# Kernel tuning notes

Hardware: AMD Instinct MI355X
Metric: run time of the kernel (lower is better)

## Reference

```python
import jax, jax.numpy as jnp
import numpy as np

WB = 8   # weight bit width (signed int8, power-of-two scale)
AB = 8   # activation bit width (uint8, power-of-two scale)
BB = 8   # bias bit width

# (name, c_in, c_out, kernel) for every QuantConv2d in order
_CFG = [("1", 3, 32, 3), ("2", 32, 16, 3), ("31", 16, 16, 1), ("32", 16, 32, 3),
        ("33", 32, 32, 1), ("34", 32, 64, 3), ("41", 64, 32, 1), ("42", 32, 64, 3),
        ("43", 64, 32, 1), ("44", 32, 64, 3), ("45", 64, 32, 1), ("46", 32, 64, 3)]
_POOL_AFTER = {"1", "2", "34"}  # MaxPool2d(2,2) follows these blocks


def _ste_round(x):
    # straight-through rounding (Brevitas-style fake quant)
    return x + jax.lax.stop_gradient(jnp.round(x) - x)


def _p2_scale(maxv, levels):
    # power-of-two (fixed point) per-tensor scale covering maxv with `levels` steps
    maxv = jnp.maximum(jax.lax.stop_gradient(maxv), 1e-8)
    return 2.0 ** jnp.ceil(jnp.log2(maxv / levels))


def quant_int(x, bw):
    # signed symmetric fixed-point fake quant (Int8WeightPerTensorFixedPoint style)
    n = 2.0 ** (bw - 1) - 1.0
    s = _p2_scale(jnp.max(jnp.abs(x)), n)
    return jnp.clip(_ste_round(x / s), -n - 1.0, n) * s


def quant_uint(x, bw):
    # unsigned fixed-point fake quant (Uint8ActPerTensorFixedPoint style)
    n = 2.0 ** bw - 1.0
    s = _p2_scale(jnp.max(x), n)
    return jnp.clip(_ste_round(x / s), 0.0, n) * s


def _conv(x, w, pad):
    return jax.lax.conv_general_dilated(
        x, w, window_strides=(1, 1), padding=[(pad, pad), (pad, pad)],
        dimension_numbers=("NCHW", "OIHW", "NCHW"))


def _maxpool2(x):
    return jax.lax.reduce_window(x, -jnp.inf, jax.lax.max,
                                 (1, 1, 2, 2), (1, 1, 2, 2), "VALID")


def _forward(x, p):
    # QuantIdentity on input (uint8 fixed point)
    x = quant_uint(x, AB)
    for n, ci, co, k in _CFG:
        pad = (k - 1) // 2
        y = _conv(x, quant_int(p["w" + n], WB), pad)               # quantized conv, no bias
        # BatchNorm2dToQuantScaleBias: per-channel affine with quantized scale/bias
        y = (y * quant_int(p["sg" + n], WB)[None, :, None, None]
             + quant_int(p["sb" + n], BB)[None, :, None, None])
        x = quant_uint(jax.nn.relu(y), AB)                          # QuantReLU
        if n in _POOL_AFTER:
            x = _maxpool2(x)
    # TruncAvgPool2d(28,28) over the remaining 28x28 map + RoundTo8bit requant
    x = quant_uint(jnp.mean(x, axis=(2, 3)), 8)                     # [B, 64]
    h = x @ quant_int(p["fw1"], WB).T + quant_int(p["fb1"], BB)     # linear51
    h = quant_uint(jax.nn.relu(h), AB)                              # relu5
    return h @ quant_int(p["fw2"], WB).T + quant_int(p["fb2"], BB)  # linear52


def setup_inputs() -> dict:
    key = jax.random.key(0)
    ks = iter(jax.random.split(key, 64))
    inp = {"x": jax.random.uniform(next(ks), (16, 3, 224, 224), jnp.float32)}
    for n, ci, co, k in _CFG:
        inp["w" + n] = jax.random.normal(next(ks), (co, ci, k, k), jnp.float32) * 0.1
        inp["sg" + n] = jax.random.uniform(next(ks), (co,), jnp.float32, 0.5, 1.5)
        inp["sb" + n] = jax.random.normal(next(ks), (co,), jnp.float32) * 0.1
    inp["fw1"] = jax.random.normal(next(ks), (16, 64), jnp.float32) * 0.1
    inp["fb1"] = jax.random.normal(next(ks), (16,), jnp.float32) * 0.1
    inp["fw2"] = jax.random.normal(next(ks), (10, 16), jnp.float32) * 0.1
    inp["fb2"] = jax.random.normal(next(ks), (10,), jnp.float32) * 0.1
    return inp


def reference(x, w1, sg1, sb1, w2, sg2, sb2, w31, sg31, sb31, w32, sg32, sb32,
              w33, sg33, sb33, w34, sg34, sb34, w41, sg41, sb41, w42, sg42, sb42,
              w43, sg43, sb43, w44, sg44, sb44, w45, sg45, sb45, w46, sg46, sb46,
              fw1, fb1, fw2, fb2):
    p = dict(locals())
    x = p.pop("x")
    return _forward(x, p)
```

## Files before the change

### kernel.cpp

```cpp
#include <hip/hip_runtime.h>
#include <math.h>

#define NL 12

typedef short v8s __attribute__((ext_vector_type(8)));
typedef float v4f __attribute__((ext_vector_type(4)));

struct PrepArgs {
  const float* in[40];
  void* out[40];
  int n[40];
  int mode[40];
  int tc[40];
  int ci[40], kk[40], kp[40], co[40];
};

__device__ inline float p2_scale_f(float maxv, float levels) {
  float r = __fdiv_rn(fmaxf(maxv, 1e-8f), levels);
  unsigned b = __float_as_uint(r);
  unsigned e = (b >> 23) & 0xffu;
  e += (b & 0x7fffffu) ? 1u : 0u;
  return __uint_as_float(e << 23);
}

__device__ inline float p2_inv(float s) {
  return __uint_as_float((254u << 23) - __float_as_uint(s));
}

__device__ inline float block_reduce_max256(float v) {
  __shared__ float sm[4];
  #pragma unroll
  for (int off = 32; off; off >>= 1) v = fmaxf(v, __shfl_down(v, off));
  if ((threadIdx.x & 63) == 0) sm[threadIdx.x >> 6] = v;
  __syncthreads();
  if (threadIdx.x == 0) v = fmaxf(fmaxf(sm[0], sm[1]), fmaxf(sm[2], sm[3]));
  return v;
}

__device__ inline void slot_max_update(float* slot, float v) {
  volatile unsigned int* su = (volatile unsigned int*)slot;
  unsigned int bits = __float_as_uint(v);
  if (bits > *su) atomicMax((unsigned int*)slot, bits);
}

__device__ inline short ibf16(float v) {
  return (short)(__float_as_uint(v) >> 16);
}

__global__ void prep_kernel(PrepArgs a, float* wslot,
                            const float* __restrict__ x, int nx, float* slot0) {
  if (blockIdx.x >= 40) {
    const float4* xv = (const float4*)x;
    const int nv = nx >> 2;
    float m0 = 0.f, m1 = 0.f, m2 = 0.f, m3 = 0.f;
    for (int i = (blockIdx.x - 40) * 256 + threadIdx.x; i < nv;
         i += (gridDim.x - 40) * 256) {
      float4 v = xv[i];
      m0 = fmaxf(m0, v.x); m1 = fmaxf(m1, v.y);
      m2 = fmaxf(m2, v.z); m3 = fmaxf(m3, v.w);
    }
    float m = fmaxf(fmaxf(m0, m1), fmaxf(m2, m3));
    float bm = block_reduce_max256(m);
    if (threadIdx.x == 0) slot_max_update(slot0, bm);
    return;
  }
  __shared__ float ssc;
  const int t = blockIdx.x;
  const float* in = a.in[t];
  const int n = a.n[t], mode = a.mode[t];
  float m = 0.f;
  if (mode >= 2) {
    const float4* in4 = (const float4*)in;
    const int n4 = n >> 2;
    for (int i = threadIdx.x; i < n4; i += 256) {
      float4 v = in4[i];
      m = fmaxf(m, fmaxf(fmaxf(fabsf(v.x), fabsf(v.y)),
                         fmaxf(fabsf(v.z), fabsf(v.w))));
    }
  } else {
    for (int i = threadIdx.x; i < n; i += 256) m = fmaxf(m, fabsf(in[i]));
  }
  float bm = block_reduce_max256(m);
  if (threadIdx.x == 0) {
    ssc = p2_scale_f(bm, 127.0f);
    if (mode >= 2) wslot[t] = ssc;
  }
  __syncthreads();
  const float s = ssc;
  if (mode == 3) {
    ushort* o = (ushort*)a.out[t];
    for (int i = threadIdx.x; i < 32 * 64; i += 256) {
      int co = i >> 6, k = i & 63;
      int khkw = k >> 2, ci = k & 3;
      ushort v = 0;
      if (khkw < 9 && ci < 3) {
        float q = rintf(__fdiv_rn(in[(co * 3 + ci) * 9 + khkw], s));
        q = fminf(fmaxf(q, -128.f), 127.f);
        v = (ushort)(__float_as_uint(q) >> 16);
      }
      o[i] = v;
    }
  } else if (mode == 2) {
    ushort* o = (ushort*)a.out[t];
    const int CI = a.ci[t], KK = a.kk[t], KP = a.kp[t], CO = a.co[t];
    const int KT = CI * KK;
    for (int i = threadIdx.x; i < CO * KP; i += 256) {
      int co = i / KP, k = i % KP;
      ushort v = 0;
      if (k < KT) {
        int khkw = k / CI, ci = k % CI;
        float q = rintf(__fdiv_rn(in[(co * CI + ci) * KK + khkw], s));
        q = fminf(fmaxf(q, -128.f), 127.f);
        v = (ushort)(__float_as_uint(q) >> 16);
      }
      o[i] = v;
    }
  } else {
    float* o = (float*)a.out[t];
    const int tc = a.tc[t];
    const int nw = (mode == 1) ? n / tc : 1;
    for (int i = threadIdx.x; i < n; i += 256) {
      float q = rintf(__fdiv_rn(in[i], s));
      q = fminf(fmaxf(q, -128.f), 127.f);
      float v = __fmul_rn(q, s);
      if (mode == 1) o[(i % nw) * tc + i / nw] = v;
      else o[i] = v;
    }
  }
}


template <int CI, int H, int CO, bool POOL, int TOUT>
__global__ __launch_bounds__(256)
void conv_lds(const float* __restrict__ in, const short* __restrict__ wt,
              const float* __restrict__ sg, const float* __restrict__ sb,
              float* __restrict__ out, const float* __restrict__ slot_in,
              const float* __restrict__ wslotp, float* slot_out) {
  constexpr int W = H;
  constexpr int KT = 9 * CI;
  constexpr int SLABS = (KT + 31) / 32;
  constexpr int KP = SLABS * 32;
  constexpr int COT = CO / 16;
  constexpr int TIN = TOUT + 2;
  constexpr int NTL = (H + TOUT - 1) / TOUT;
  constexpr int PT = TOUT / 4;
  constexpr int NP = (PT * PT) / 4;
  constexpr int HO = POOL ? H / 2 : H;
  constexpr int WO = POOL ? W / 2 : W;
  constexpr int LG = (CI == 16) ? 2 : 3;
  constexpr int CH = CI / 4;

  __shared__ ushort lds[TIN * TIN * CI];

  auto lidx = [](int pix, int cs) -> int {
    if constexpr (CI == 32) return pix * CI + (cs ^ ((pix & 3) << 3));
    else return pix * CI + cs;
  };

  const int lane = threadIdx.x & 63, widx = threadIdx.x >> 6;
  const int quad = lane >> 4, col = lane & 15;
  const float s_in = p2_scale_f(slot_in[0], 255.0f);
  const float inv = p2_inv(s_in);
  const float S = __fmul_rn(s_in, wslotp[0]);

  const int bt = blockIdx.x;
  const int n = bt / (NTL * NTL);
  const int rr = bt % (NTL * NTL);
  const int ty = rr / NTL, tx = rr % NTL;
  const int gh0 = ty * TOUT - 1, gw0 = tx * TOUT - 1;
  const float* ib = in + (size_t)n * H * W * CI;

  for (int i = threadIdx.x; i < TIN * TIN * CH; i += 256) {
    const int pix = i >> LG, cg = i & (CH - 1);
    const int hi = pix / TIN, wi = pix - hi * TIN;
    const int gh = gh0 + hi, gw = gw0 + wi;
    float4 f = {0.f, 0.f, 0.f, 0.f};
    if ((unsigned)gh < (unsigned)H && (unsigned)gw < (unsigned)W)
      f = *(const float4*)(ib + ((size_t)(gh * W + gw)) * CI + cg * 4);
    ushort4 c;
    c.x = (ushort)ibf16(rintf(__fmul_rn(f.x, inv)));
    c.y = (ushort)ibf16(rintf(__fmul_rn(f.y, inv)));
    c.z = (ushort)ibf16(rintf(__fmul_rn(f.z, inv)));
    c.w = (ushort)ibf16(rintf(__fmul_rn(f.w, inv)));
    *(ushort4*)(lds + lidx(pix, cg * 4)) = c;
  }
  __syncthreads();

  v4f acc[NP][COT];
  #pragma unroll
  for (int p = 0; p < NP; p++)
    #pragma unroll
    for (int c = 0; c < COT; c++) acc[p][c] = (v4f){0.f, 0.f, 0.f, 0.f};

  #pragma unroll
  for (int slab = 0; slab < SLABS; slab++) {
    const int kbase = slab * 32 + quad * 8;
    int tap = kbase / CI; tap = min(tap, 8);
    const int cib = kbase % CI;
    const int kh = tap / 3, kw = tap - kh * 3;
    v8s b[COT];
    #pragma unroll
    for (int c = 0; c < COT; c++)
      b[c] = *(const v8s*)(wt + (size_t)(c * 16 + col) * KP + kbase);
    #pragma unroll
    for (int p = 0; p < NP; p++) {
      const int q = widx * NP + p;
      const int plh = (q / PT) * 4, plw = (q % PT) * 4;
      const int hin = plh + (col >> 2) + kh, win = plw + (col & 3) + kw;
      v8s a = *(const v8s*)(lds + lidx(hin * TIN + win, cib));
      #pragma unroll
      for (int c = 0; c < COT; c++)
        acc[p][c] = __builtin_amdgcn_mfma_f32_16x16x32_bf16(a, b[c], acc[p][c], 0, 0, 0);
    }
  }

  float zmax = 0.f;
  #pragma unroll
  for (int p = 0; p < NP; p++) {
    const int q = widx * NP + p;
    const int plh = (q / PT) * 4, plw = (q % PT) * 4;
    const int gho = ty * TOUT + plh, gwo = tx * TOUT + plw;
    #pragma unroll
    for (int c = 0; c < COT; c++) {
      const int cog = c * 16 + col;
      const float g = sg[cog], bb = sb[cog];
      float z[4];
      #pragma unroll
      for (int r2 = 0; r2 < 4; r2++) {
        float t = __fmul_rn(acc[p][c][r2], S);
        z[r2] = fmaxf(__fadd_rn(__fmul_rn(t, g), bb), 0.f);
      }
      if constexpr (POOL) {
        float h0 = fmaxf(z[0], z[1]), h1 = fmaxf(z[2], z[3]);
        float o0 = fmaxf(h0, __shfl_xor(h0, 16));
        float o1 = fmaxf(h1, __shfl_xor(h1, 16));
        const int oh = (gho >> 1) + (quad >> 1), ow = gwo >> 1;
        const bool v0 = (oh < HO) && (ow < WO), v1 = (oh < HO) && (ow + 1 < WO);
        zmax = fmaxf(zmax, fmaxf(v0 ? o0 : 0.f, v1 ? o1 : 0.f));
        if (!(quad & 1)) {
          float* op = out + ((size_t)((n * HO + oh) * WO + ow)) * CO + cog;
          if (v0) op[0] = o0;
          if (v1) op[CO] = o1;
        }
      } else {
        const int hh = gho + quad;
        #pragma unroll
        for (int r2 = 0; r2 < 4; r2++) {
          const int wwo = gwo + r2;
          if (hh < H && wwo < W) {
            out[(size_t)((n * H + hh) * W + wwo) * CO + cog] = z[r2];
            zmax = fmaxf(zmax, z[r2]);
          }
        }
      }
    }
  }
  float bm = block_reduce_max256(zmax);
  if (threadIdx.x == 0) slot_max_update(slot_out, bm);
}

__global__ __launch_bounds__(256)
void conv1_lds(const float* __restrict__ x, const short* __restrict__ wt,
               const float* __restrict__ sg, const float* __restrict__ sb,
               float* __restrict__ out, const float* __restrict__ slot_in,
               const float* __restrict__ wslotp, float* slot_out) {
  constexpr int H = 224, W = 224, CO = 32, TOUT = 16, TIN = 18, NTL = 14;
  constexpr int HO = 112, WO = 112;
  __shared__ ushort lds[TIN * TIN * 4];

  const int lane = threadIdx.x & 63, widx = threadIdx.x >> 6;
  const int quad = lane >> 4, col = lane & 15;
  const float s_in = p2_scale_f(slot_in[0], 255.0f);
  const float inv = p2_inv(s_in);
  const float S = __fmul_rn(s_in, wslotp[0]);

  const int bt = blockIdx.x;
  const int n = bt / (NTL * NTL);
  const int rr = bt % (NTL * NTL);
  const int ty = rr / NTL, tx = rr % NTL;
  const int gh0 = ty * TOUT - 1, gw0 = tx * TOUT - 1;
  const float* xb = x + (size_t)n * 3 * H * W;

  for (int i = threadIdx.x; i < 3 * TIN * TIN; i += 256) {
    const int c = i / (TIN * TIN), pix = i - c * TIN * TIN;
    const int hi = pix / TIN, wi = pix - hi * TIN;
    const int gh = gh0 + hi, gw = gw0 + wi;
    ushort code = 0;
    if ((unsigned)gh < (unsigned)H && (unsigned)gw < (unsigned)W)
      code = (ushort)ibf16(rintf(__fmul_rn(xb[(size_t)c * H * W + gh * W + gw], inv)));
    lds[pix * 4 + c] = code;
  }
  for (int i = threadIdx.x; i < TIN * TIN; i += 256) lds[i * 4 + 3] = 0;
  __syncthreads();

  const int plh = (widx >> 1) * 8, plwq = (widx & 1) * 8;
  v4f acc[4][2];
  #pragma unroll
  for (int p = 0; p < 4; p++) { acc[p][0] = (v4f){0,0,0,0}; acc[p][1] = acc[p][0]; }

  auto read4 = [&](int ph, int pw, int tap) -> ushort4 {
    const int hin = ph + (col >> 2) + tap / 3, win = pw + (col & 3) + tap % 3;
    return ((const ushort4*)lds)[hin * TIN + win];
  };

  #pragma unroll
  for (int slab = 0; slab < 2; slab++) {
    const int kbase = slab * 32 + quad * 8;
    int tA = slab * 8 + quad * 2; int tB = tA + 1;
    tA = min(tA, 8); tB = min(tB, 8);
    v8s b0 = *(const v8s*)(wt + (size_t)(col) * 64 + kbase);
    v8s b1 = *(const v8s*)(wt + (size_t)(16 + col) * 64 + kbase);
    #pragma unroll
    for (int p = 0; p < 4; p++) {
      const int ph = plh + (p >> 1) * 4, pw = plwq + (p & 1) * 4;
      ushort4 lo = read4(ph, pw, tA);
      ushort4 hi = read4(ph, pw, tB);
      v8s a;
      a[0] = (short)lo.x; a[1] = (short)lo.y; a[2] = (short)lo.z; a[3] = (short)lo.w;
      a[4] = (short)hi.x; a[5] = (short)hi.y; a[6] = (short)hi.z; a[7] = (short)hi.w;
      acc[p][0] = __builtin_amdgcn_mfma_f32_16x16x32_bf16(a, b0, acc[p][0], 0, 0, 0);
      acc[p][1] = __builtin_amdgcn_mfma_f32_16x16x32_bf16(a, b1, acc[p][1], 0, 0, 0);
    }
  }

  float zmax = 0.f;
  #pragma unroll
  for (int p = 0; p < 4; p++) {
    const int gho = ty * TOUT + plh + (p >> 1) * 4;
    const int gwo = tx * TOUT + plwq + (p & 1) * 4;
    #pragma unroll
    for (int c = 0; c < 2; c++) {
      const int cog = c * 16 + col;
      const float g = sg[cog], bb = sb[cog];
      float z[4];
      #pragma unroll
      for (int r2 = 0; r2 < 4; r2++) {
        float t = __fmul_rn(acc[p][c][r2], S);
        z[r2] = fmaxf(__fadd_rn(__fmul_rn(t, g), bb), 0.f);
      }
      float h0 = fmaxf(z[0], z[1]), h1 = fmaxf(z[2], z[3]);
      float o0 = fmaxf(h0, __shfl_xor(h0, 16));
      float o1 = fmaxf(h1, __shfl_xor(h1, 16));
      zmax = fmaxf(zmax, fmaxf(o0, o1));
      if (!(quad & 1)) {
        const int oh = (gho >> 1) + (quad >> 1), ow = gwo >> 1;
        float* op = out + ((size_t)((n * HO + oh) * WO + ow)) * CO + cog;
        op[0] = o0; op[CO] = o1;
      }
    }
  }
  float bm = block_reduce_max256(zmax);
  if (threadIdx.x == 0) slot_max_update(slot_out, bm);
}

template <int CI, int H, int CO, bool K3, bool POOL, int CSPLIT>
__global__ __launch_bounds__(256)
void conv_mfma(const float* __restrict__ in, const short* __restrict__ wt,
               const float* __restrict__ sg, const float* __restrict__ sb,
               float* __restrict__ out, const float* __restrict__ slot_in,
               const float* __restrict__ wslotp, float* slot_out) {
  constexpr int W = H;
  constexpr int KT = (K3 ? 9 : 1) * CI;
  constexpr int SLABS = (KT + 31) / 32;
  constexpr int KP = SLABS * 32;
  constexpr int COT = CO / (16 * CSPLIT);
  constexpr int HO = POOL ? H / 2 : H;
  constexpr int WO = POOL ? W / 2 : W;

  const int lane = threadIdx.x & 63, widx = threadIdx.x >> 6;
  const int quad = lane >> 4, col = lane & 15;
  const float s_in = p2_scale_f(slot_in[0], 255.0f);
  const float inv = p2_inv(s_in);
  const float S = __fmul_rn(s_in, wslotp[0]);
  const int wv = blockIdx.x * 4 + widx;
  const int mt = wv / CSPLIT, ct = wv % CSPLIT;

  int n, h, w, ph = 0, pw = 0;
  if constexpr (POOL) {
    constexpr int PB = (HO / 2) * (WO / 2);
    n = mt / PB; int r = mt % PB;
    ph = r / (WO / 2); pw = r % (WO / 2);
    h = 4 * ph + (col >> 2); w = 4 * pw + (col & 3);
  } else {
    int p = mt * 16 + col;
    n = p / (H * W); int r = p % (H * W);
    h = r / W; w = r % W;
  }
  const float* ibase = in + (size_t)n * H * W * CI;

  float4 fa[SLABS], fb[SLABS];
  bool vm[SLABS];
  #pragma unroll
  for (int slab = 0; slab < SLABS; slab++) {
    const int kbase = slab * 32 + quad * 8;
    const float* ap;
    if constexpr (K3) {
      const int khkw = min(kbase / CI, 8);
      const int cib = kbase % CI;
      const int kh = khkw / 3, kw = khkw - kh * 3;
      const int hh = h + kh - 1, ww = w + kw - 1;
      vm[slab] = (hh >= 0) && (hh < H) && (ww >= 0) && (ww < W);
      const int hc = min(max(hh, 0), H - 1), wc = min(max(ww, 0), W - 1);
      ap = ibase + (size_t)(hc * W + wc) * CI + cib;
    } else {
      vm[slab] = true;
      ap = ibase + (size_t)(h * W + w) * CI + (kbase % CI);
    }
    fa[slab] = ((const float4*)ap)[0];
    fb[slab] = ((const float4*)ap)[1];
  }

  v4f acc[COT];
  #pragma unroll
  for (int c = 0; c < COT; c++) acc[c] = (v4f){0.f, 0.f, 0.f, 0.f};

  #pragma unroll
  for (int slab = 0; slab < SLABS; slab++) {
    const int kbase = slab * 32 + quad * 8;
    float ff[8] = {fa[slab].x, fa[slab].y, fa[slab].z, fa[slab].w,
                   fb[slab].x, fb[slab].y, fb[slab].z, fb[slab].w};
    v8s a;
    #pragma unroll
    for (int j = 0; j < 8; j++) {
      float q = rintf(__fmul_rn(ff[j], inv));
      a[j] = vm[slab] ? ibf16(q) : (short)0;
    }
    #pragma unroll
    for (int c = 0; c < COT; c++) {
      v8s b = *(const v8s*)(wt + (size_t)((ct * COT + c) * 16 + col) * KP + kbase);
      acc[c] = __builtin_amdgcn_mfma_f32_16x16x32_bf16(a, b, acc[c], 0, 0, 0);
    }
  }

  float zmax = 0.f;
  #pragma unroll
  for (int c = 0; c < COT; c++) {
    const int cog = (ct * COT + c) * 16 + col;
    const float g = sg[cog], bb = sb[cog];
    float z[4];
    #pragma unroll
    for (int r2 = 0; r2 < 4; r2++) {
      float t = __fmul_rn(acc[c][r2], S);
      z[r2] = fmaxf(__fadd_rn(__fmul_rn(t, g), bb), 0.f);
    }
    if constexpr (POOL) {
      float h0 = fmaxf(z[0], z[1]), h1 = fmaxf(z[2], z[3]);
      float o0 = fmaxf(h0, __shfl_xor(h0, 16));
      float o1 = fmaxf(h1, __shfl_xor(h1, 16));
      zmax = fmaxf(zmax, fmaxf(o0, o1));
      if (!(quad & 1)) {
        int oh = 2 * ph + (quad >> 1), ow = 2 * pw;
        float* op = out + ((size_t)((n * HO + oh) * WO + ow)) * CO + cog;
        op[0] = o0; op[CO] = o1;
      }
    } else {
      const int pbase = mt * 16 + quad * 4;
      #pragma unroll
      for (int r2 = 0; r2 < 4; r2++) {
        out[(size_t)(pbase + r2) * CO + cog] = z[r2];
        zmax = fmaxf(zmax, z[r2]);
      }
    }
  }
  float bm = block_reduce_max256(zmax);
  if (threadIdx.x == 0) slot_max_update(slot_out, bm);
}

__global__ void avgpool_kernel(const float* __restrict__ in, float* __restrict__ out,
                               const float* __restrict__ slot_in, float* slot_out) {
  __shared__ float red[1024];
  const float s = p2_scale_f(slot_in[0], 255.0f);
  const float inv = p2_inv(s);
  const int nn = blockIdx.x, co = threadIdx.x & 63, part = threadIdx.x >> 6;
  const float* p = in + (size_t)nn * 784 * 64;
  float sum = 0.f;
  for (int i = part * 49; i < part * 49 + 49; i++)
    sum += __fmul_rn(rintf(__fmul_rn(p[i * 64 + co], inv)), s);
  red[threadIdx.x] = sum;
  __syncthreads();
  if (threadIdx.x < 64) {
    float tot = 0.f;
    #pragma unroll
    for (int k2 = 0; k2 < 16; k2++) tot += red[k2 * 64 + co];
    float m = __fdiv_rn(tot, 784.0f);
    out[nn * 64 + co] = m;
    slot_max_update(slot_out, m);
  }
}

__global__ void tail_kernel(const float* __restrict__ pooled,
                            const float* __restrict__ fw1, const float* __restrict__ fb1,
                            const float* __restrict__ fw2, const float* __restrict__ fb2,
                            const float* __restrict__ slot_in, float* __restrict__ out) {
  __shared__ float xq[1024];
  __shared__ float hq[256];
  __shared__ float s2s;
  const int t = threadIdx.x;
  const float s = p2_scale_f(slot_in[0], 255.0f);
  const float inv = p2_inv(s);
  for (int i = t; i < 1024; i += 256)
    xq[i] = __fmul_rn(rintf(__fmul_rn(pooled[i], inv)), s);
  __syncthreads();
  const int n = t >> 4, j = t & 15;
  float acc = 0.f;
  #pragma unroll 8
  for (int k = 0; k < 64; k++) acc += xq[n * 64 + k] * fw1[k * 16 + j];
  float z = fmaxf(__fadd_rn(acc, fb1[j]), 0.f);
  float bm = block_reduce_max256(z);
  if (t == 0) s2s = p2_scale_f(bm, 255.0f);
  __syncthreads();
  const float s2 = s2s, inv2 = p2_inv(s2);
  hq[t] = __fmul_rn(rintf(__fmul_rn(z, inv2)), s2);
  __syncthreads();
  if (t < 160) {
    const int n2 = t / 10, j2 = t % 10;
    float a2 = 0.f;
    #pragma unroll
    for (int k = 0; k < 16; k++) a2 += hq[n2 * 16 + k] * fw2[k * 10 + j2];
    out[t] = __fadd_rn(a2, fb2[j2]);
  }
}

extern "C" void kernel_launch(void* const* d_in, const int* in_sizes, int n_in,
                              void* d_out, int out_size, void* d_ws, size_t ws_size,
                              hipStream_t stream) {
  static const int h_ci[NL] = {3, 32, 16, 16, 32, 32, 64, 32, 64, 32, 64, 32};
  static const int h_co[NL] = {32, 16, 16, 32, 32, 64, 32, 64, 32, 64, 32, 64};
  static const int h_kk[NL] = {9, 9, 1, 9, 1, 9, 1, 9, 1, 9, 1, 9};
  static const int h_kp[NL] = {64, 288, 32, 160, 32, 288, 64, 288, 64, 288, 64, 288};

  float* ws = (float*)d_ws;
  float* slots = ws;
  float* wslot = ws + 16;
  size_t off = 32;

  short* wq[NL];
  for (int l = 0; l < NL; l++) {
    wq[l] = (short*)(ws + off);
    off += (size_t)(h_co[l] * h_kp[l] + 1) / 2;
  }
  float* sgq[NL]; float* sbq[NL];
  for (int l = 0; l < NL; l++) { sgq[l] = ws + off; off += 64; }
  for (int l = 0; l < NL; l++) { sbq[l] = ws + off; off += 64; }
  float* fw1q = ws + off; off += 1024;
  float* fb1q = ws + off; off += 16;
  float* fw2q = ws + off; off += 160;
  float* fb2q = ws + off; off += 16;
  float* A = ws + off; off += 6422528;
  float* B = ws + off; off += 1605632;
  float* P = ws + off; off += 1024;

  PrepArgs pa;
  for (int l = 0; l < NL; l++) {
    pa.in[l] = (const float*)d_in[1 + 3 * l]; pa.out[l] = (void*)wq[l];
    pa.n[l] = h_co[l] * h_ci[l] * h_kk[l];
    pa.mode[l] = (l == 0) ? 3 : 2; pa.tc[l] = 0;
    pa.ci[l] = h_ci[l]; pa.kk[l] = h_kk[l]; pa.kp[l] = h_kp[l]; pa.co[l] = h_co[l];
    pa.in[12 + l] = (const float*)d_in[2 + 3 * l]; pa.out[12 + l] = (void*)sgq[l];
    pa.n[12 + l] = h_co[l]; pa.mode[12 + l] = 0; pa.tc[12 + l] = 0;
    pa.ci[12 + l] = pa.kk[12 + l] = pa.kp[12 + l] = pa.co[12 + l] = 0;
    pa.in[24 + l] = (const float*)d_in[3 + 3 * l]; pa.out[24 + l] = (void*)sbq[l];
    pa.n[24 + l] = h_co[l]; pa.mode[24 + l] = 0; pa.tc[24 + l] = 0;
    pa.ci[24 + l] = pa.kk[24 + l] = pa.kp[24 + l] = pa.co[24 + l] = 0;
  }
  pa.in[36] = (const float*)d_in[37]; pa.out[36] = (void*)fw1q;
  pa.n[36] = 1024; pa.mode[36] = 1; pa.tc[36] = 16;
  pa.ci[36] = pa.kk[36] = pa.kp[36] = pa.co[36] = 0;
  pa.in[37] = (const float*)d_in[38]; pa.out[37] = (void*)fb1q;
  pa.n[37] = 16; pa.mode[37] = 0; pa.tc[37] = 0;
  pa.ci[37] = pa.kk[37] = pa.kp[37] = pa.co[37] = 0;
  pa.in[38] = (const float*)d_in[39]; pa.out[38] = (void*)fw2q;
  pa.n[38] = 160; pa.mode[38] = 1; pa.tc[38] = 10;
  pa.ci[38] = pa.kk[38] = pa.kp[38] = pa.co[38] = 0;
  pa.in[39] = (const float*)d_in[40]; pa.out[39] = (void*)fb2q;
  pa.n[39] = 10; pa.mode[39] = 0; pa.tc[39] = 0;
  pa.ci[39] = pa.kk[39] = pa.kp[39] = pa.co[39] = 0;

  const float* x = (const float*)d_in[0];
  const int nx = 16 * 3 * 224 * 224;

  hipMemsetAsync(slots, 0, 16 * sizeof(float), stream);
  prep_kernel<<<40 + 294, 256, 0, stream>>>(pa, wslot, x, nx, slots + 0);

  conv1_lds<<<16 * 14 * 14, 256, 0, stream>>>(x, wq[0], sgq[0], sbq[0], A,
                                              slots + 0, wslot + 0, slots + 1);
  conv_lds<32, 112, 16, true, 16><<<16 * 49, 256, 0, stream>>>(
      A, wq[1], sgq[1], sbq[1], B, slots + 1, wslot + 1, slots + 2);
  conv_mfma<16, 56, 16, false, false, 1><<<784, 256, 0, stream>>>(
      B, wq[2], sgq[2], sbq[2], A, slots + 2, wslot + 2, slots + 3);
  conv_lds<16, 56, 32, false, 16><<<16 * 16, 256, 0, stream>>>(
      A, wq[3], sgq[3], sbq[3], B, slots + 3, wslot + 3, slots + 4);
  conv_mfma<32, 56, 32, false, false, 2><<<1568, 256, 0, stream>>>(
      B, wq[4], sgq[4], sbq[4], A, slots + 4, wslot + 4, slots + 5);
  conv_lds<32, 56, 64, true, 16><<<16 * 16, 256, 0, stream>>>(
      A, wq[5], sgq[5], sbq[5], B, slots + 5, wslot + 5, slots + 6);
  conv_mfma<64, 28, 32, false, false, 2><<<392, 256, 0, stream>>>(
      B, wq[6], sgq[6], sbq[6], A, slots + 6, wslot + 6, slots + 7);
  conv_lds<32, 28, 64, false, 8><<<16 * 16, 256, 0, stream>>>(
      A, wq[7], sgq[7], sbq[7], B, slots + 7, wslot + 7, slots + 8);
  conv_mfma<64, 28, 32, false, false, 2><<<392, 256, 0, stream>>>(
      B, wq[8], sgq[8], sbq[8], A, slots + 8, wslot + 8, slots + 9);
  conv_lds<32, 28, 64, false, 8><<<16 * 16, 256, 0, stream>>>(
      A, wq[9], sgq[9], sbq[9], B, slots + 9, wslot + 9, slots + 10);
  conv_mfma<64, 28, 32, false, false, 2><<<392, 256, 0, stream>>>(
      B, wq[10], sgq[10], sbq[10], A, slots + 10, wslot + 10, slots + 11);
  conv_lds<32, 28, 64, false, 8><<<16 * 16, 256, 0, stream>>>(
      A, wq[11], sgq[11], sbq[11], B, slots + 11, wslot + 11, slots + 12);

  avgpool_kernel<<<16, 1024, 0, stream>>>(B, P, slots + 12, slots + 13);
  tail_kernel<<<1, 256, 0, stream>>>(P, fw1q, fb1q, fw2q, fb2q, slots + 13,
                                     (float*)d_out);
}
```

Baseline: 330.6 us.

## Enlarge conv1 tiles, hoist weight fragments, and use per-wave atomic max

conv1 now uses 32x32 output tiles (34x34 input halo) with 784 blocks instead of 16x16 tiles with 3136. This cuts halo reloads and per-block overhead. Weight fragments are loaded once into registers, and each wave loops over sixteen 4x4 patches. The block-level max reduction (shared memory plus syncthreads) is replaced by a wave shuffle reduction followed by a per-wave atomicMax, which adds atomic traffic. The pooled conv_mfma path also changes its index from mt to wv, which alters the pooled index mapping.

```diff
diff --git a/kernel.cpp b/kernel.cpp
--- a/kernel.cpp
+++ b/kernel.cpp
@@ -41,6 +41,12 @@
   volatile unsigned int* su = (volatile unsigned int*)slot;
   unsigned int bits = __float_as_uint(v);
   if (bits > *su) atomicMax((unsigned int*)slot, bits);
+}
+
+__device__ inline void wave_max_update(float v, float* slot) {
+  #pragma unroll
+  for (int off = 32; off; off >>= 1) v = fmaxf(v, __shfl_down(v, off));
+  if ((threadIdx.x & 63) == 0) slot_max_update(slot, v);
 }
 
 __device__ inline short ibf16(float v) {
@@ -60,8 +66,7 @@
       m2 = fmaxf(m2, v.z); m3 = fmaxf(m3, v.w);
     }
     float m = fmaxf(fmaxf(m0, m1), fmaxf(m2, m3));
-    float bm = block_reduce_max256(m);
-    if (threadIdx.x == 0) slot_max_update(slot0, bm);
+    wave_max_update(m, slot0);
     return;
   }
   __shared__ float ssc;
@@ -255,8 +260,7 @@
       }
     }
   }
-  float bm = block_reduce_max256(zmax);
-  if (threadIdx.x == 0) slot_max_update(slot_out, bm);
+  wave_max_update(zmax, slot_out);
 }
 
 __global__ __launch_bounds__(256)
@@ -264,7 +268,7 @@
                const float* __restrict__ sg, const float* __restrict__ sb,
                float* __restrict__ out, const float* __restrict__ slot_in,
                const float* __restrict__ wslotp, float* slot_out) {
-  constexpr int H = 224, W = 224, CO = 32, TOUT = 16, TIN = 18, NTL = 14;
+  constexpr int H = 224, W = 224, CO = 32, TOUT = 32, TIN = 34, NTL = 7;
   constexpr int HO = 112, WO = 112;
   __shared__ ushort lds[TIN * TIN * 4];
 
@@ -282,7 +286,7 @@
   const float* xb = x + (size_t)n * 3 * H * W;
 
   for (int i = threadIdx.x; i < 3 * TIN * TIN; i += 256) {
-    const int c = i / (TIN * TIN), pix = i - c * TIN * TIN;
+    const int c = i / (TIN * TIN), pix = i - c * (TIN * TIN);
     const int hi = pix / TIN, wi = pix - hi * TIN;
     const int gh = gh0 + hi, gw = gw0 + wi;
     ushort code = 0;
@@ -293,41 +297,42 @@
   for (int i = threadIdx.x; i < TIN * TIN; i += 256) lds[i * 4 + 3] = 0;
   __syncthreads();
 
-  const int plh = (widx >> 1) * 8, plwq = (widx & 1) * 8;
-  v4f acc[4][2];
-  #pragma unroll
-  for (int p = 0; p < 4; p++) { acc[p][0] = (v4f){0,0,0,0}; acc[p][1] = acc[p][0]; }
+  v8s bfr[2][2];
+  #pragma unroll
+  for (int slab = 0; slab < 2; slab++) {
+    bfr[slab][0] = *(const v8s*)(wt + (size_t)(col) * 64 + slab * 32 + quad * 8);
+    bfr[slab][1] = *(const v8s*)(wt + (size_t)(16 + col) * 64 + slab * 32 + quad * 8);
+  }
+  const int t0A = min(quad * 2, 8),     t0B = min(quad * 2 + 1, 8);
+  const int t1A = min(8 + quad * 2, 8), t1B = min(8 + quad * 2 + 1, 8);
 
   auto read4 = [&](int ph, int pw, int tap) -> ushort4 {
     const int hin = ph + (col >> 2) + tap / 3, win = pw + (col & 3) + tap % 3;
     return ((const ushort4*)lds)[hin * TIN + win];
   };
-
-  #pragma unroll
-  for (int slab = 0; slab < 2; slab++) {
-    const int kbase = slab * 32 + quad * 8;
-    int tA = slab * 8 + quad * 2; int tB = tA + 1;
-    tA = min(tA, 8); tB = min(tB, 8);
-    v8s b0 = *(const v8s*)(wt + (size_t)(col) * 64 + kbase);
-    v8s b1 = *(const v8s*)(wt + (size_t)(16 + col) * 64 + kbase);
-    #pragma unroll
-    for (int p = 0; p < 4; p++) {
-      const int ph = plh + (p >> 1) * 4, pw = plwq + (p & 1) * 4;
-      ushort4 lo = read4(ph, pw, tA);
-      ushort4 hi = read4(ph, pw, tB);
-      v8s a;
-      a[0] = (short)lo.x; a[1] = (short)lo.y; a[2] = (short)lo.z; a[3] = (short)lo.w;
-      a[4] = (short)hi.x; a[5] = (short)hi.y; a[6] = (short)hi.z; a[7] = (short)hi.w;
-      acc[p][0] = __builtin_amdgcn_mfma_f32_16x16x32_bf16(a, b0, acc[p][0], 0, 0, 0);
-      acc[p][1] = __builtin_amdgcn_mfma_f32_16x16x32_bf16(a, b1, acc[p][1], 0, 0, 0);
-    }
-  }
+  auto mka = [](ushort4 lo, ushort4 hi) -> v8s {
+    v8s a;
+    a[0] = (short)lo.x; a[1] = (short)lo.y; a[2] = (short)lo.z; a[3] = (short)lo.w;
+    a[4] = (short)hi.x; a[5] = (short)hi.y; a[6] = (short)hi.z; a[7] = (short)hi.w;
+    return a;
+  };
 
   float zmax = 0.f;
-  #pragma unroll
-  for (int p = 0; p < 4; p++) {
-    const int gho = ty * TOUT + plh + (p >> 1) * 4;
-    const int gwo = tx * TOUT + plwq + (p & 1) * 4;
+  for (int p = widx; p < 64; p += 4) {
+    const int plh = (p >> 3) * 4, plw = (p & 7) * 4;
+    v4f acc[2];
+    acc[0] = (v4f){0.f, 0.f, 0.f, 0.f}; acc[1] = acc[0];
+    {
+      v8s a = mka(read4(plh, plw, t0A), read4(plh, plw, t0B));
+      acc[0] = __builtin_amdgcn_mfma_f32_16x16x32_bf16(a, bfr[0][0], acc[0], 0, 0, 0);
+      acc[1] = __builtin_amdgcn_mfma_f32_16x16x32_bf16(a, bfr[0][1], acc[1], 0, 0, 0);
+    }
+    {
+      v8s a = mka(read4(plh, plw, t1A), read4(plh, plw, t1B));
+      acc[0] = __builtin_amdgcn_mfma_f32_16x16x32_bf16(a, bfr[1][0], acc[0], 0, 0, 0);
+      acc[1] = __builtin_amdgcn_mfma_f32_16x16x32_bf16(a, bfr[1][1], acc[1], 0, 0, 0);
+    }
+    const int gho = ty * TOUT + plh, gwo = tx * TOUT + plw;
     #pragma unroll
     for (int c = 0; c < 2; c++) {
       const int cog = c * 16 + col;
@@ -335,7 +340,7 @@
       float z[4];
       #pragma unroll
       for (int r2 = 0; r2 < 4; r2++) {
-        float t = __fmul_rn(acc[p][c][r2], S);
+        float t = __fmul_rn(acc[c][r2], S);
         z[r2] = fmaxf(__fadd_rn(__fmul_rn(t, g), bb), 0.f);
       }
       float h0 = fmaxf(z[0], z[1]), h1 = fmaxf(z[2], z[3]);
@@ -349,8 +354,7 @@
       }
     }
   }
-  float bm = block_reduce_max256(zmax);
-  if (threadIdx.x == 0) slot_max_update(slot_out, bm);
+  wave_max_update(zmax, slot_out);
 }
 
 template <int CI, int H, int CO, bool K3, bool POOL, int CSPLIT>
@@ -378,7 +382,7 @@
   int n, h, w, ph = 0, pw = 0;
   if constexpr (POOL) {
     constexpr int PB = (HO / 2) * (WO / 2);
-    n = mt / PB; int r = mt % PB;
+    n = wv / PB; int r = wv % PB;
     ph = r / (WO / 2); pw = r % (WO / 2);
     h = 4 * ph + (col >> 2); w = 4 * pw + (col & 3);
   } else {
@@ -462,8 +466,7 @@
       }
     }
   }
-  float bm = block_reduce_max256(zmax);
-  if (threadIdx.x == 0) slot_max_update(slot_out, bm);
+  wave_max_update(zmax, slot_out);
 }
 
 __global__ void avgpool_kernel(const float* __restrict__ in, float* __restrict__ out,
@@ -582,8 +585,8 @@
   hipMemsetAsync(slots, 0, 16 * sizeof(float), stream);
   prep_kernel<<<40 + 294, 256, 0, stream>>>(pa, wslot, x, nx, slots + 0);
 
-  conv1_lds<<<16 * 14 * 14, 256, 0, stream>>>(x, wq[0], sgq[0], sbq[0], A,
-                                              slots + 0, wslot + 0, slots + 1);
+  conv1_lds<<<16 * 7 * 7, 256, 0, stream>>>(x, wq[0], sgq[0], sbq[0], A,
+                                            slots + 0, wslot + 0, slots + 1);
   conv_lds<32, 112, 16, true, 16><<<16 * 49, 256, 0, stream>>>(
       A, wq[1], sgq[1], sbq[1], B, slots + 1, wslot + 1, slots + 2);
   conv_mfma<16, 56, 16, false, false, 1><<<784, 256, 0, stream>>>(
```

Result: slower. 502.3 us (+51.9%).
